# Performance work log

Hardware: AMD Instinct MI355X
Metric: run time of the kernel (lower is better)

The kernel has to match this reference:

```python
import jax, jax.numpy as jnp
import numpy as np
from jax import lax

# Fixed-point scales (powers of two, as in linger's luna/venus pipeline).
# scale_gi = input_scale * weight_ih_scale, scale_gh = hidden_scale * weight_hh_scale.
SCALE_GI = 2.0 ** 14
SCALE_GH = 2.0 ** 14
Q27 = 2.0 ** 27
Q15 = 2.0 ** 15
Q31 = 2.0 ** 31
INT32_MIN = -(2.0 ** 31)
INT32_MAX = 2.0 ** 31 - 1


def quant_round(x, scale):
    # QuantMode.floor_add: floor(x*scale + 0.5)/scale, with straight-through gradient
    # (linger QAT rounding uses STE).
    q = jnp.floor(x * scale + 0.5) / scale
    return x + lax.stop_gradient(q - x)


@jax.custom_vjp
def qsigmoid(x):
    # Quantize input to Q27 int32, evaluate sigmoid, output Q31 -> requant to Q15.
    i_q27 = jnp.clip(jnp.floor(x * Q27 + 0.5), INT32_MIN, INT32_MAX)
    s = jax.nn.sigmoid(i_q27 / Q27)
    out_q31 = jnp.floor(s * Q31 + 0.5)
    out_q15 = jnp.floor(out_q31 * (2.0 ** -16) + 0.5)  # luna_requant(31 -> 15)
    return out_q15 / Q15

def _qsig_fwd(x):
    return qsigmoid(x), x

def _qsig_bwd(x, g):
    s = jax.nn.sigmoid(x)
    return (g * s * (1.0 - s),)

qsigmoid.defvjp(_qsig_fwd, _qsig_bwd)


@jax.custom_vjp
def qtanh(x):
    i_q27 = jnp.clip(jnp.floor(x * Q27 + 0.5), INT32_MIN, INT32_MAX)
    t = jnp.tanh(i_q27 / Q27)
    out_q31 = jnp.floor(t * Q31 + 0.5)
    out_q15 = jnp.floor(out_q31 * (2.0 ** -16) + 0.5)
    return out_q15 / Q15

def _qtanh_fwd(x):
    return qtanh(x), x

def _qtanh_bwd(x, g):
    t = jnp.tanh(x)
    return (g * (1.0 - t * t),)

qtanh.defvjp(_qtanh_fwd, _qtanh_bwd)


def setup_inputs() -> dict:
    key = jax.random.key(0)
    k = jax.random.split(key, 6)
    B, I, H = 8192, 512, 512
    return {
        "input_x": jax.random.normal(k[0], (B, I), dtype=jnp.float32),
        "hidden": jax.random.normal(k[1], (B, H), dtype=jnp.float32),
        "weight_ih": jax.random.normal(k[2], (3 * H, I), dtype=jnp.float32) * 0.05,
        "weight_hh": jax.random.normal(k[3], (3 * H, H), dtype=jnp.float32) * 0.05,
        "bias_ih": jax.random.normal(k[4], (3 * H,), dtype=jnp.float32) * 0.05,
        "bias_hh": jax.random.normal(k[5], (3 * H,), dtype=jnp.float32) * 0.05,
    }


def reference(input_x, hidden, weight_ih, weight_hh, bias_ih, bias_hh):
    # Dense gate projections: [B, 3H]
    gi = input_x @ weight_ih.T + bias_ih
    gh = hidden @ weight_hh.T + bias_hh
    # Requant gate pre-activations to fixed-point grid (biasih/biashh quantizers)
    gi = quant_round(gi, SCALE_GI)
    gh = quant_round(gh, SCALE_GH)
    i_r, i_i, i_n = jnp.split(gi, 3, axis=1)
    h_r, h_i, h_n = jnp.split(gh, 3, axis=1)
    resetgate = qsigmoid(i_r + h_r)
    inputgate = qsigmoid(i_i + h_i)
    # h_n requantized to Q27, reset*h_n product requantized to Q15
    h_n = quant_round(h_n, Q27)
    resetgate_h_n = quant_round(resetgate * h_n, Q15)
    newgate = qtanh(resetgate_h_n + i_n)
    new_hidden = quant_round(hidden, Q15)
    hy = newgate + inputgate * (new_hidden - newgate)
    return hy
```

## Files before the change

kernel.cpp:

```cpp
#include <hip/hip_runtime.h>
#include <math.h>


typedef _Float16 f16x8  __attribute__((ext_vector_type(8)));
typedef __bf16   bf16x8 __attribute__((ext_vector_type(8)));
typedef float    f32x16 __attribute__((ext_vector_type(16)));

namespace {

constexpr int Bsz = 8192, Ksz = 512, Hsz = 512;
constexpr int BM = 64, BN = 64, KT = 32;

constexpr unsigned WCH0    = 16384u;
constexpr unsigned WS_F16  = (16384u + 3072u) * 512u;
constexpr size_t   WS_NEED = (size_t)WS_F16 * 2;

__device__ __forceinline__ float qround(float x, float s, float invs) {
    return floorf(x * s + 0.5f) * invs;
}

__device__ __forceinline__ float qsigmoid_dev(float x) {
    float iq = floorf(x * 134217728.0f + 0.5f);
    iq = fminf(fmaxf(iq, -2147483648.0f), 2147483648.0f);
    float e = __expf(-iq * 7.450580596923828125e-9f);
    float s = __builtin_amdgcn_rcpf(1.0f + e);
    float q31 = floorf(s * 2147483648.0f + 0.5f);
    float q15 = floorf(q31 * 1.52587890625e-5f + 0.5f);
    return q15 * 3.0517578125e-5f;
}

__device__ __forceinline__ float qtanh_dev(float x) {
    float iq = floorf(x * 134217728.0f + 0.5f);
    iq = fminf(fmaxf(iq, -2147483648.0f), 2147483648.0f);
    float z = iq * 7.450580596923828125e-9f;
    float e = __expf(2.0f * z);
    float t = 1.0f - 2.0f * __builtin_amdgcn_rcpf(e + 1.0f);
    float q31 = floorf(t * 2147483648.0f + 0.5f);
    float q15 = floorf(q31 * 1.52587890625e-5f + 0.5f);
    return q15 * 3.0517578125e-5f;
}

__device__ __forceinline__ void dma16(const void* g, void* l) {
    __builtin_amdgcn_global_load_lds(
        (const __attribute__((address_space(1))) unsigned int*)g,
        (__attribute__((address_space(3))) unsigned int*)l, 16, 0, 0);
}

__device__ __forceinline__ void split2(float a, float b, unsigned& hi, unsigned& lo) {
    unsigned ua = __float_as_uint(a); ua += 0x7fffu + ((ua >> 16) & 1u);
    unsigned ub = __float_as_uint(b); ub += 0x7fffu + ((ub >> 16) & 1u);
    hi = (ua >> 16) | (ub & 0xffff0000u);
    float ra = a - __uint_as_float(ua & 0xffff0000u);
    float rb = b - __uint_as_float(ub & 0xffff0000u);
    unsigned va = __float_as_uint(ra); va += 0x7fffu + ((va >> 16) & 1u);
    unsigned vb = __float_as_uint(rb); vb += 0x7fffu + ((vb >> 16) & 1u);
    lo = (va >> 16) | (vb & 0xffff0000u);
}

}

__global__ __launch_bounds__(256) void cvt_tile_f16(
    const float* __restrict__ x, const float* __restrict__ h,
    const float* __restrict__ wih, const float* __restrict__ whh,
    _Float16* __restrict__ ws)
{
    const int row  = blockIdx.x * 4 + (threadIdx.x >> 6);
    const int lane = threadIdx.x & 63;
    const float* src;
    unsigned chunk0;
    unsigned rin;
    if (row < 8192) {
        src = x + (size_t)row * 512;
        chunk0 = (unsigned)(row >> 5) * 32u;
        rin = row & 31;
    } else if (row < 16384) {
        int r = row - 8192;
        src = h + (size_t)r * 512;
        chunk0 = 8192u + (unsigned)(r >> 5) * 32u;
        rin = r & 31;
    } else {
        int w = row - 16384;
        int g, n;
        if (w < 1536) { g = w >> 9;        n = w & 511;  src = wih + (size_t)w * 512; }
        else { int v = w - 1536; g = 3 + (v >> 9); n = v & 511; src = whh + (size_t)v * 512; }
        chunk0 = WCH0 + (unsigned)((g * 16 + (n >> 5)) * 32);
        rin = n & 31;
    }
    const int K16 = lane >> 1, kh = lane & 1;
    float4 v0 = *(const float4*)(src + lane * 8);
    float4 v1 = *(const float4*)(src + lane * 8 + 4);
    f16x8 o;
    o[0] = (_Float16)v0.x; o[1] = (_Float16)v0.y;
    o[2] = (_Float16)v0.z; o[3] = (_Float16)v0.w;
    o[4] = (_Float16)v1.x; o[5] = (_Float16)v1.y;
    o[6] = (_Float16)v1.z; o[7] = (_Float16)v1.w;
    *(f16x8*)(ws + (size_t)(chunk0 + K16) * 512u + kh * 256 + rin * 8) = o;
}

__global__ __launch_bounds__(256, 2) void qgru_f16_dma2(
    const _Float16* __restrict__ ws, const float* __restrict__ hid,
    const float* __restrict__ bih, const float* __restrict__ bhh,
    float* __restrict__ out)
{
    __shared__ __align__(16) _Float16 lds[32768];

    const int t = threadIdx.x, lane = t & 63, wid = t >> 6;
    const int mt = wid >> 1, nt = wid & 1;
    const int m0 = blockIdx.x * BM, n0 = blockIdx.y * BN;

    unsigned goff[8];
    int      ldst[8];
    if (wid == 0) {
#pragma unroll
        for (int c = 0; c < 8; ++c) {
            int arr = c >> 2, mtc = (c >> 1) & 1, ks2 = c & 1;
            unsigned ch = (unsigned)arr * 8192u
                        + (unsigned)((m0 >> 5) + mtc) * 32u + (unsigned)ks2;
            goff[c] = ch * 1024u + (unsigned)lane * 16u;
            ldst[c] = (arr * 2 + mtc) * 1024 + ks2 * 512;
        }
    } else {
#pragma unroll
        for (int c = 0; c < 8; ++c) {
            int g = (wid - 1) * 2 + (c >> 2), ntc = (c >> 1) & 1, ks2 = c & 1;
            unsigned ch = WCH0
                        + (unsigned)((g * 16 + (n0 >> 5) + ntc) * 32) + (unsigned)ks2;
            goff[c] = ch * 1024u + (unsigned)lane * 16u;
            ldst[c] = 4096 + (g * 2 + ntc) * 1024 + ks2 * 512;
        }
    }

    f32x16 acc[6];
#pragma unroll
    for (int g = 0; g < 6; ++g)
#pragma unroll
        for (int i = 0; i < 16; ++i) acc[g][i] = 0.0f;

    const char* wsb = (const char*)ws;
    const int lr = lane & 31, lk8 = (lane >> 5) * 8;

#pragma unroll
    for (int c = 0; c < 8; ++c)
        dma16(wsb + goff[c], &lds[ldst[c]]);

    for (int step = 0; step < 16; ++step) {
        __syncthreads();

        if (step + 1 < 16) {
            const unsigned kb = (unsigned)(step + 1) * 2048u;
            const int nb = ((step + 1) & 1) * 16384;
#pragma unroll
            for (int c = 0; c < 8; ++c)
                dma16(wsb + goff[c] + kb, &lds[nb + ldst[c]]);
        }

        const int cb = (step & 1) * 16384;
#pragma unroll
        for (int ks2 = 0; ks2 < 2; ++ks2) {
            const int lfo = cb + ks2 * 512 + lk8 * 32 + lr * 8;
            const f16x8 ax = *(const f16x8*)&lds[lfo + (0 + mt) * 1024];
            const f16x8 ah = *(const f16x8*)&lds[lfo + (2 + mt) * 1024];
#pragma unroll
            for (int g = 0; g < 6; ++g) {
                const f16x8 b = *(const f16x8*)&lds[lfo + 4096 + (g * 2 + nt) * 1024];
                acc[g] = __builtin_amdgcn_mfma_f32_32x32x16_f16(
                             g < 3 ? ax : ah, b, acc[g], 0, 0, 0);
            }
        }
    }

    constexpr float S14 = 16384.0f,     I14 = 1.0f / 16384.0f;
    constexpr float S15 = 32768.0f,     I15 = 1.0f / 32768.0f;
    constexpr float S27 = 134217728.0f, I27 = 1.0f / 134217728.0f;

    const int lh = lane >> 5, l32 = lane & 31;
    const int n = n0 + nt * 32 + l32;
    const float br = bih[n], bi = bih[n + 512], bn = bih[n + 1024];
    const float cr = bhh[n], ci = bhh[n + 512], cn = bhh[n + 1024];

#pragma unroll
    for (int r = 0; r < 16; ++r) {
        const int row = (r & 3) + 8 * (r >> 2) + 4 * lh;
        const int m   = m0 + mt * 32 + row;
        const float hv = hid[(size_t)m * Hsz + n];

        float gir = qround(acc[0][r] + br, S14, I14);
        float gii = qround(acc[1][r] + bi, S14, I14);
        float gin = qround(acc[2][r] + bn, S14, I14);
        float ghr = qround(acc[3][r] + cr, S14, I14);
        float ghi = qround(acc[4][r] + ci, S14, I14);
        float ghn = qround(acc[5][r] + cn, S14, I14);
        float resetg = qsigmoid_dev(gir + ghr);
        float inputg = qsigmoid_dev(gii + ghi);
        float hn  = qround(ghn, S27, I27);
        float rh  = qround(resetg * hn, S15, I15);
        float newg = qtanh_dev(rh + gin);
        float nh  = qround(hv, S15, I15);
        out[(size_t)m * Hsz + n] = newg + inputg * (nh - newg);
    }
}

__global__ __launch_bounds__(256, 2) void qgru_mfma_bf16x3(
    const float* __restrict__ x, const float* __restrict__ hid,
    const float* __restrict__ wih, const float* __restrict__ whh,
    const float* __restrict__ bih, const float* __restrict__ bhh,
    float* __restrict__ out)
{
    __shared__ __align__(16) unsigned short lds[16384];

    const int t = threadIdx.x, lane = t & 63, wid = t >> 6;
    const int mt = wid >> 1, nt = wid & 1;
    const int m0 = blockIdx.x * BM, n0 = blockIdx.y * BN;
    const int s_r = t >> 2, s_k = (t & 3) << 2;
    const int s_kh = s_k >> 3, s_j = s_k & 7, s_rt = s_r >> 5, s_r32 = s_r & 31;

    const float* gA[2];
    gA[0] = x   + (size_t)(m0 + s_r) * Ksz + s_k;
    gA[1] = hid + (size_t)(m0 + s_r) * Ksz + s_k;
    const float* gW[6];
#pragma unroll
    for (int g = 0; g < 3; ++g) {
        gW[g]     = wih + (size_t)(g * Hsz + n0 + s_r) * Ksz + s_k;
        gW[g + 3] = whh + (size_t)(g * Hsz + n0 + s_r) * Ksz + s_k;
    }
    const int lh = lane >> 5, l32 = lane & 31;

    f32x16 acc[6];
#pragma unroll
    for (int g = 0; g < 6; ++g)
#pragma unroll
        for (int i = 0; i < 16; ++i) acc[g][i] = 0.0f;

    float4 vA[2], vW[6];
#pragma unroll
    for (int tt = 0; tt < 2; ++tt) vA[tt] = *(const float4*)gA[tt];
#pragma unroll
    for (int g = 0; g < 6; ++g)    vW[g]  = *(const float4*)gW[g];

    for (int k0 = 0; k0 < Ksz; k0 += 16) {
        __syncthreads();
#pragma unroll
        for (int tt = 0; tt < 2; ++tt) {
            unsigned h0, h1, l0, l1;
            split2(vA[tt].x, vA[tt].y, h0, l0);
            split2(vA[tt].z, vA[tt].w, h1, l1);
            unsigned bH = ((((tt*2+0)*2+s_rt)*2+s_kh)*32+s_r32)*8 + s_j;
            unsigned bL = ((((tt*2+1)*2+s_rt)*2+s_kh)*32+s_r32)*8 + s_j;
            *reinterpret_cast<uint2*>(&lds[bH]) = make_uint2(h0, h1);
            *reinterpret_cast<uint2*>(&lds[bL]) = make_uint2(l0, l1);
        }
#pragma unroll
        for (int g = 0; g < 6; ++g) {
            unsigned h0, h1, l0, l1;
            split2(vW[g].x, vW[g].y, h0, l0);
            split2(vW[g].z, vW[g].w, h1, l1);
            unsigned bH = 4096u + ((((g*2+0)*2+s_rt)*2+s_kh)*32+s_r32)*8 + s_j;
            unsigned bL = 4096u + ((((g*2+1)*2+s_rt)*2+s_kh)*32+s_r32)*8 + s_j;
            *reinterpret_cast<uint2*>(&lds[bH]) = make_uint2(h0, h1);
            *reinterpret_cast<uint2*>(&lds[bL]) = make_uint2(l0, l1);
        }
        __syncthreads();
        const int kn = (k0 + 16 < Ksz) ? (k0 + 16) : 0;
#pragma unroll
        for (int tt = 0; tt < 2; ++tt) vA[tt] = *(const float4*)(gA[tt] + kn);
#pragma unroll
        for (int g = 0; g < 6; ++g)    vW[g]  = *(const float4*)(gW[g] + kn);

        const bf16x8 ax_hi = *reinterpret_cast<const bf16x8*>(&lds[((((0)*2+mt)*2+lh)*32+l32)*8]);
        const bf16x8 ax_lo = *reinterpret_cast<const bf16x8*>(&lds[((((1)*2+mt)*2+lh)*32+l32)*8]);
        const bf16x8 ah_hi = *reinterpret_cast<const bf16x8*>(&lds[((((2)*2+mt)*2+lh)*32+l32)*8]);
        const bf16x8 ah_lo = *reinterpret_cast<const bf16x8*>(&lds[((((3)*2+mt)*2+lh)*32+l32)*8]);
#pragma unroll
        for (int g = 0; g < 6; ++g) {
            const bf16x8 b_hi = *reinterpret_cast<const bf16x8*>(&lds[4096u + ((((g*2+0)*2+nt)*2+lh)*32+l32)*8]);
            const bf16x8 b_lo = *reinterpret_cast<const bf16x8*>(&lds[4096u + ((((g*2+1)*2+nt)*2+lh)*32+l32)*8]);
            const bf16x8 a_hi = (g < 3) ? ax_hi : ah_hi;
            const bf16x8 a_lo = (g < 3) ? ax_lo : ah_lo;
            acc[g] = __builtin_amdgcn_mfma_f32_32x32x16_bf16(a_hi, b_hi, acc[g], 0, 0, 0);
            acc[g] = __builtin_amdgcn_mfma_f32_32x32x16_bf16(a_hi, b_lo, acc[g], 0, 0, 0);
            acc[g] = __builtin_amdgcn_mfma_f32_32x32x16_bf16(a_lo, b_hi, acc[g], 0, 0, 0);
        }
    }

    constexpr float S14 = 16384.0f,     I14 = 1.0f / 16384.0f;
    constexpr float S15 = 32768.0f,     I15 = 1.0f / 32768.0f;
    constexpr float S27 = 134217728.0f, I27 = 1.0f / 134217728.0f;
    const int n = n0 + nt * 32 + l32;
    const float br = bih[n], bi = bih[n + 512], bn = bih[n + 1024];
    const float cr = bhh[n], ci = bhh[n + 512], cn = bhh[n + 1024];
#pragma unroll
    for (int r = 0; r < 16; ++r) {
        const int row = (r & 3) + 8 * (r >> 2) + 4 * lh;
        const int m   = m0 + mt * 32 + row;
        const float hv = hid[(size_t)m * Hsz + n];
        float gir = qround(acc[0][r] + br, S14, I14);
        float gii = qround(acc[1][r] + bi, S14, I14);
        float gin = qround(acc[2][r] + bn, S14, I14);
        float ghr = qround(acc[3][r] + cr, S14, I14);
        float ghi = qround(acc[4][r] + ci, S14, I14);
        float ghn = qround(acc[5][r] + cn, S14, I14);
        float resetg = qsigmoid_dev(gir + ghr);
        float inputg = qsigmoid_dev(gii + ghi);
        float hn  = qround(ghn, S27, I27);
        float rh  = qround(resetg * hn, S15, I15);
        float newg = qtanh_dev(rh + gin);
        float nh  = qround(hv, S15, I15);
        out[(size_t)m * Hsz + n] = newg + inputg * (nh - newg);
    }
}

extern "C" void kernel_launch(void* const* d_in, const int* in_sizes, int n_in,
                              void* d_out, int out_size, void* d_ws, size_t ws_size,
                              hipStream_t stream) {
    const float* x   = (const float*)d_in[0];
    const float* hid = (const float*)d_in[1];
    const float* wih = (const float*)d_in[2];
    const float* whh = (const float*)d_in[3];
    const float* bih = (const float*)d_in[4];
    const float* bhh = (const float*)d_in[5];
    float* out = (float*)d_out;
    dim3 grid(Bsz / BM, Hsz / BN);

    if (ws_size >= WS_NEED) {
        cvt_tile_f16<<<19456 / 4, 256, 0, stream>>>(x, hid, wih, whh, (_Float16*)d_ws);
        qgru_f16_dma2<<<grid, dim3(256), 0, stream>>>(
            (const _Float16*)d_ws, hid, bih, bhh, out);
    } else {
        qgru_mfma_bf16x3<<<grid, dim3(256), 0, stream>>>(
            x, hid, wih, whh, bih, bhh, out);
    }
}
```

Before: 131.9 us.

## Halve K-step LDS tile for higher occupancy and gather-style fp16 conversion

The GEMM kernel now stages one 16-wide K slice per step instead of two. This halves LDS use to 32 KB and raises the launch-bounds occupancy hint from 2 to 3 blocks, at the cost of twice as many barriers and DMA rounds. The conversion kernel is rewritten so each wave writes contiguous 1 KB output chunks by gathering strided fp32 reads, instead of reading contiguous rows and scattering fp16 writes. Both changes aim to improve latency hiding and write coalescing, but the smaller K step cuts the MFMA work available between synchronizations.

```diff
diff --git a/kernel.cpp b/kernel.cpp
--- a/kernel.cpp
+++ b/kernel.cpp
@@ -9,10 +9,11 @@
 namespace {
 
 constexpr int Bsz = 8192, Ksz = 512, Hsz = 512;
-constexpr int BM = 64, BN = 64, KT = 32;
+constexpr int BM = 64, BN = 64;
 
 constexpr unsigned WCH0    = 16384u;
-constexpr unsigned WS_F16  = (16384u + 3072u) * 512u;
+constexpr unsigned NCHUNK  = 16384u + 3072u;
+constexpr unsigned WS_F16  = NCHUNK * 512u;
 constexpr size_t   WS_NEED = (size_t)WS_F16 * 2;
 
 __device__ __forceinline__ float qround(float x, float s, float invs) {
@@ -59,74 +60,77 @@
 
 }
 
-__global__ __launch_bounds__(256) void cvt_tile_f16(
+__global__ __launch_bounds__(256) void cvt_gather_f16(
     const float* __restrict__ x, const float* __restrict__ h,
     const float* __restrict__ wih, const float* __restrict__ whh,
     _Float16* __restrict__ ws)
 {
-    const int row  = blockIdx.x * 4 + (threadIdx.x >> 6);
+    const int wid  = threadIdx.x >> 6;
     const int lane = threadIdx.x & 63;
-    const float* src;
-    unsigned chunk0;
-    unsigned rin;
-    if (row < 8192) {
-        src = x + (size_t)row * 512;
-        chunk0 = (unsigned)(row >> 5) * 32u;
-        rin = row & 31;
-    } else if (row < 16384) {
-        int r = row - 8192;
-        src = h + (size_t)r * 512;
-        chunk0 = 8192u + (unsigned)(r >> 5) * 32u;
-        rin = r & 31;
-    } else {
-        int w = row - 16384;
-        int g, n;
-        if (w < 1536) { g = w >> 9;        n = w & 511;  src = wih + (size_t)w * 512; }
-        else { int v = w - 1536; g = 3 + (v >> 9); n = v & 511; src = whh + (size_t)v * 512; }
-        chunk0 = WCH0 + (unsigned)((g * 16 + (n >> 5)) * 32);
-        rin = n & 31;
-    }
-    const int K16 = lane >> 1, kh = lane & 1;
-    float4 v0 = *(const float4*)(src + lane * 8);
-    float4 v1 = *(const float4*)(src + lane * 8 + 4);
-    f16x8 o;
-    o[0] = (_Float16)v0.x; o[1] = (_Float16)v0.y;
-    o[2] = (_Float16)v0.z; o[3] = (_Float16)v0.w;
-    o[4] = (_Float16)v1.x; o[5] = (_Float16)v1.y;
-    o[6] = (_Float16)v1.z; o[7] = (_Float16)v1.w;
-    *(f16x8*)(ws + (size_t)(chunk0 + K16) * 512u + kh * 256 + rin * 8) = o;
-}
-
-__global__ __launch_bounds__(256, 2) void qgru_f16_dma2(
+    const unsigned c0 = (blockIdx.x * 4u + wid) * 4u;
+    const int r32  = lane & 31;
+    const int koct = (lane >> 5) * 8;
+
+#pragma unroll
+    for (int i = 0; i < 4; ++i) {
+        const unsigned c = c0 + i;
+        const float* src;
+        unsigned K16;
+        if (c < WCH0) {
+            const unsigned arr = c >> 13, rel = c & 8191u;
+            const unsigned M32 = rel >> 5;
+            K16 = rel & 31u;
+            src = (arr ? h : x) + (size_t)(M32 * 32 + r32) * 512u;
+        } else {
+            const unsigned rel = c - WCH0;
+            K16 = rel & 31u;
+            const unsigned gn32 = rel >> 5;
+            const unsigned g = gn32 >> 4, N32 = gn32 & 15u;
+            const unsigned rowLocal = (g % 3u) * 512u + N32 * 32u + r32;
+            src = (g < 3 ? wih : whh) + (size_t)rowLocal * 512u;
+        }
+        const float* p = src + K16 * 16 + koct;
+        float4 v0 = *(const float4*)p;
+        float4 v1 = *(const float4*)(p + 4);
+        f16x8 o;
+        o[0] = (_Float16)v0.x; o[1] = (_Float16)v0.y;
+        o[2] = (_Float16)v0.z; o[3] = (_Float16)v0.w;
+        o[4] = (_Float16)v1.x; o[5] = (_Float16)v1.y;
+        o[6] = (_Float16)v1.z; o[7] = (_Float16)v1.w;
+        *(f16x8*)(ws + (size_t)c * 512u + lane * 8) = o;
+    }
+}
+
+__global__ __launch_bounds__(256, 3) void qgru_f16_kt16(
     const _Float16* __restrict__ ws, const float* __restrict__ hid,
     const float* __restrict__ bih, const float* __restrict__ bhh,
     float* __restrict__ out)
 {
-    __shared__ __align__(16) _Float16 lds[32768];
+    __shared__ __align__(16) _Float16 lds[16384];
 
     const int t = threadIdx.x, lane = t & 63, wid = t >> 6;
     const int mt = wid >> 1, nt = wid & 1;
     const int m0 = blockIdx.x * BM, n0 = blockIdx.y * BN;
 
-    unsigned goff[8];
-    int      ldst[8];
+    unsigned goff[4];
+    int      ldst[4];
     if (wid == 0) {
 #pragma unroll
-        for (int c = 0; c < 8; ++c) {
-            int arr = c >> 2, mtc = (c >> 1) & 1, ks2 = c & 1;
-            unsigned ch = (unsigned)arr * 8192u
-                        + (unsigned)((m0 >> 5) + mtc) * 32u + (unsigned)ks2;
+        for (int c = 0; c < 4; ++c) {
+            const int arr = c >> 1, mtc = c & 1;
+            const unsigned ch = (unsigned)arr * 8192u
+                              + (unsigned)((m0 >> 5) + mtc) * 32u;
             goff[c] = ch * 1024u + (unsigned)lane * 16u;
-            ldst[c] = (arr * 2 + mtc) * 1024 + ks2 * 512;
+            ldst[c] = c * 512;
         }
     } else {
 #pragma unroll
-        for (int c = 0; c < 8; ++c) {
-            int g = (wid - 1) * 2 + (c >> 2), ntc = (c >> 1) & 1, ks2 = c & 1;
-            unsigned ch = WCH0
-                        + (unsigned)((g * 16 + (n0 >> 5) + ntc) * 32) + (unsigned)ks2;
+        for (int c = 0; c < 4; ++c) {
+            const int g = (wid - 1) * 2 + (c >> 1), ntc = c & 1;
+            const unsigned ch = WCH0
+                              + (unsigned)((g * 16 + (n0 >> 5) + ntc) * 32);
             goff[c] = ch * 1024u + (unsigned)lane * 16u;
-            ldst[c] = 4096 + (g * 2 + ntc) * 1024 + ks2 * 512;
+            ldst[c] = 2048 + (g * 2 + ntc) * 512;
         }
     }
 
@@ -137,35 +141,31 @@
         for (int i = 0; i < 16; ++i) acc[g][i] = 0.0f;
 
     const char* wsb = (const char*)ws;
-    const int lr = lane & 31, lk8 = (lane >> 5) * 8;
-
-#pragma unroll
-    for (int c = 0; c < 8; ++c)
+    const int lfo = (lane >> 5) * 256 + (lane & 31) * 8;
+
+#pragma unroll
+    for (int c = 0; c < 4; ++c)
         dma16(wsb + goff[c], &lds[ldst[c]]);
 
-    for (int step = 0; step < 16; ++step) {
+    for (int step = 0; step < 32; ++step) {
         __syncthreads();
 
-        if (step + 1 < 16) {
-            const unsigned kb = (unsigned)(step + 1) * 2048u;
-            const int nb = ((step + 1) & 1) * 16384;
-#pragma unroll
-            for (int c = 0; c < 8; ++c)
+        if (step + 1 < 32) {
+            const unsigned kb = (unsigned)(step + 1) * 1024u;
+            const int nb = ((step + 1) & 1) * 8192;
+#pragma unroll
+            for (int c = 0; c < 4; ++c)
                 dma16(wsb + goff[c] + kb, &lds[nb + ldst[c]]);
         }
 
-        const int cb = (step & 1) * 16384;
-#pragma unroll
-        for (int ks2 = 0; ks2 < 2; ++ks2) {
-            const int lfo = cb + ks2 * 512 + lk8 * 32 + lr * 8;
-            const f16x8 ax = *(const f16x8*)&lds[lfo + (0 + mt) * 1024];
-            const f16x8 ah = *(const f16x8*)&lds[lfo + (2 + mt) * 1024];
-#pragma unroll
-            for (int g = 0; g < 6; ++g) {
-                const f16x8 b = *(const f16x8*)&lds[lfo + 4096 + (g * 2 + nt) * 1024];
-                acc[g] = __builtin_amdgcn_mfma_f32_32x32x16_f16(
-                             g < 3 ? ax : ah, b, acc[g], 0, 0, 0);
-            }
+        const int cb = (step & 1) * 8192;
+        const f16x8 ax = *(const f16x8*)&lds[cb + mt * 512 + lfo];
+        const f16x8 ah = *(const f16x8*)&lds[cb + (2 + mt) * 512 + lfo];
+#pragma unroll
+        for (int g = 0; g < 6; ++g) {
+            const f16x8 b = *(const f16x8*)&lds[cb + 2048 + (g * 2 + nt) * 512 + lfo];
+            acc[g] = __builtin_amdgcn_mfma_f32_32x32x16_f16(
+                         g < 3 ? ax : ah, b, acc[g], 0, 0, 0);
         }
     }
 
@@ -322,8 +322,9 @@
     dim3 grid(Bsz / BM, Hsz / BN);
 
     if (ws_size >= WS_NEED) {
-        cvt_tile_f16<<<19456 / 4, 256, 0, stream>>>(x, hid, wih, whh, (_Float16*)d_ws);
-        qgru_f16_dma2<<<grid, dim3(256), 0, stream>>>(
+        cvt_gather_f16<<<NCHUNK / 16, 256, 0, stream>>>(
+            x, hid, wih, whh, (_Float16*)d_ws);
+        qgru_f16_kt16<<<grid, dim3(256), 0, stream>>>(
             (const _Float16*)d_ws, hid, bih, bhh, out);
     } else {
         qgru_mfma_bf16x3<<<grid, dim3(256), 0, stream>>>(
```

Measured after the change: 138.2 us. 1.05x slower.
